# Kernel tuning notes

Hardware: AMD Instinct MI355X
Metric: run time of the kernel (lower is better)

## Reference

```python
import jax, jax.numpy as jnp
import numpy as np

B, H, W, C = 32, 56, 56, 192
WS, SHIFT, HEADS = 7, 3, 6
HID = 4 * C
N = WS * WS
NW = (H // WS) * (W // WS)
EPS = 1e-5


def _rel_index():
    ch, cw = np.meshgrid(np.arange(WS), np.arange(WS), indexing='ij')
    coords = np.stack([ch.ravel(), cw.ravel()])  # [2, N]
    rel = coords[:, :, None] - coords[:, None, :]  # [2, N, N]
    rel = rel.transpose(1, 2, 0)
    rel[:, :, 0] += WS - 1
    rel[:, :, 1] += WS - 1
    rel[:, :, 0] *= 2 * WS - 1
    return rel.sum(-1).astype(np.int32)  # [N, N]


def _attn_mask():
    img = np.zeros((H, W), np.float32)
    sl = (slice(0, -WS), slice(-WS, -SHIFT), slice(-SHIFT, None))
    cnt = 0
    for hs in sl:
        for ws_ in sl:
            img[hs, ws_] = cnt
            cnt += 1
    mw = img.reshape(H // WS, WS, W // WS, WS).transpose(0, 2, 1, 3).reshape(-1, N)
    m = mw[:, None, :] - mw[:, :, None]
    return np.where(m != 0, -100.0, 0.0).astype(np.float32)  # [NW, N, N]


def setup_inputs() -> dict:
    key = jax.random.key(0)
    ks = jax.random.split(key, 16)
    r = lambda k, s, sc: (jax.random.normal(k, s, jnp.float32) * sc)
    return {
        'x': r(ks[0], (B, H * W, C), 1.0),
        'norm1_w': jnp.ones((C,), jnp.float32),
        'norm1_b': jnp.zeros((C,), jnp.float32),
        'qkv_w': r(ks[1], (C, 3 * C), 0.02),
        'qkv_b': jnp.zeros((3 * C,), jnp.float32),
        'bias_table': r(ks[2], ((2 * WS - 1) ** 2, HEADS), 0.02),
        'proj_w': r(ks[3], (C, C), 0.02),
        'proj_b': jnp.zeros((C,), jnp.float32),
        'norm2_w': jnp.ones((C,), jnp.float32),
        'norm2_b': jnp.zeros((C,), jnp.float32),
        'fc1_w': r(ks[4], (C, HID), 0.02),
        'fc1_b': jnp.zeros((HID,), jnp.float32),
        'fc2_w': r(ks[5], (HID, C), 0.02),
        'fc2_b': jnp.zeros((C,), jnp.float32),
        'attn_mask': jnp.asarray(_attn_mask()),
        'rel_index': jnp.asarray(_rel_index()),
    }


def _ln(x, w, b):
    mu = jnp.mean(x, -1, keepdims=True)
    var = jnp.mean(jnp.square(x - mu), -1, keepdims=True)
    return (x - mu) * jax.lax.rsqrt(var + EPS) * w + b


def reference(x, norm1_w, norm1_b, qkv_w, qkv_b, bias_table, proj_w, proj_b,
              norm2_w, norm2_b, fc1_w, fc1_b, fc2_w, fc2_b, attn_mask, rel_index):
    shortcut = x
    h = _ln(x, norm1_w, norm1_b).reshape(B, H, W, C)
    # cyclic shift
    h = jnp.roll(h, shift=(-SHIFT, -SHIFT), axis=(1, 2))
    # window partition -> (B*NW, N, C)
    h = h.reshape(B, H // WS, WS, W // WS, WS, C).transpose(0, 1, 3, 2, 4, 5)
    h = h.reshape(B * NW, N, C)
    # attention
    qkv = (h @ qkv_w + qkv_b).reshape(B * NW, N, 3, HEADS, C // HEADS)
    qkv = qkv.transpose(2, 0, 3, 1, 4)  # [3, B_, heads, N, d]
    q, k, v = qkv[0], qkv[1], qkv[2]
    scale = (C // HEADS) ** -0.5
    attn = jnp.einsum('bhnd,bhmd->bhnm', q * scale, k)
    bias = bias_table[rel_index].transpose(2, 0, 1)  # [heads, N, N]
    attn = attn + bias[None]
    attn = attn.reshape(B, NW, HEADS, N, N) + attn_mask[None, :, None]
    attn = jax.nn.softmax(attn.reshape(B * NW, HEADS, N, N), axis=-1)
    o = jnp.einsum('bhnm,bhmd->bhnd', attn, v)
    o = o.transpose(0, 2, 1, 3).reshape(B * NW, N, C)
    o = o @ proj_w + proj_b
    # window reverse
    o = o.reshape(B, H // WS, W // WS, WS, WS, C).transpose(0, 1, 3, 2, 4, 5)
    o = o.reshape(B, H, W, C)
    o = jnp.roll(o, shift=(SHIFT, SHIFT), axis=(1, 2)).reshape(B, H * W, C)
    x = shortcut + o
    # MLP (exact GELU, like torch nn.GELU)
    m = _ln(x, norm2_w, norm2_b)
    m = jax.nn.gelu(m @ fc1_w + fc1_b, approximate=False) @ fc2_w + fc2_b
    return x + m
```

## Files before the change

kernel.cpp:

```cpp
#include <hip/hip_runtime.h>
#include <math.h>

#define B_    32
#define HH    56
#define WW_   56
#define C_    192
#define WS_   7
#define SHIFT_ 3
#define HEADS_ 6
#define DH    32
#define N_    49
#define NWIN  2048
#define ROWS  100352
#define HID_  768
#define QKVN  576

typedef __bf16 bfr;
typedef __bf16 bf8 __attribute__((ext_vector_type(8)));
typedef __bf16 bf4 __attribute__((ext_vector_type(4)));
typedef float  f32x4 __attribute__((ext_vector_type(4)));

#define MFMA16(a,b,c) __builtin_amdgcn_mfma_f32_16x16x32_bf16(a,b,c,0,0,0)

#define OQW   0
#define OPW   110592
#define OW1   147456
#define OW2   294912
#define OBM   442368
#define WTOT  442368
#define BMTOT 98304

__global__ __launch_bounds__(256) void k_prep(
    const float* __restrict__ qkvw, const float* __restrict__ projw,
    const float* __restrict__ w1,   const float* __restrict__ w2,
    bfr* __restrict__ wsp)
{
  int idx = blockIdx.x*256 + threadIdx.x;
  if (idx >= WTOT) return;
  if (idx < OPW)      { int i=idx;      int n=i/192, k=i%192; wsp[idx] = (bfr)qkvw[k*QKVN + n]; }
  else if (idx < OW1) { int i=idx-OPW;  int n=i/192, k=i%192; wsp[idx] = (bfr)projw[k*C_ + n]; }
  else if (idx < OW2) { int i=idx-OW1;  int n=i/192, k=i%192; wsp[idx] = (bfr)w1[k*HID_ + n]; }
  else                { int i=idx-OW2;  int n=i/768, k=i%768; wsp[idx] = (bfr)w2[k*C_ + n]; }
}

__global__ __launch_bounds__(256) void k_prep2(
    const float* __restrict__ btab, const int* __restrict__ rel,
    const float* __restrict__ mask, bfr* __restrict__ bm)
{
  int idx = blockIdx.x*256 + threadIdx.x;
  if (idx >= BMTOT) return;
  int k = idx & 63, q = (idx>>6) & 63, cls = (idx>>12) & 3, head = idx>>14;
  int wh = (cls & 2) ? 7 : 0, ww = (cls & 1) ? 7 : 0;
  int wi = wh*8 + ww;
  float v = -1e30f;
  if (q < N_ && k < N_) {
    int e = q*N_ + k;
    v = btab[rel[e]*HEADS_ + head] + mask[(size_t)wi*N_*N_ + e];
  }
  bm[idx] = (bfr)v;
}

#define SM_HS 0
#define SM_QS 25600
#define SM_KS 34816
#define SM_VT 44032
#define SM_P  53248
#define SM_OV 62464
#define SM_SR 71680
#define SM1_TOT 71936
#define HSP 200

__global__ __launch_bounds__(256, 2) void k_attn(
    const float* __restrict__ x,
    const float* __restrict__ n1w, const float* __restrict__ n1b,
    const bfr*   __restrict__ wsp,
    const float* __restrict__ qkvb,
    const float* __restrict__ projb,
    float* __restrict__ out)
{
  __shared__ char smem[SM1_TOT];
  bfr*   hs    = (bfr*)(smem + SM_HS);
  bfr*   qs    = (bfr*)(smem + SM_QS);
  bfr*   ks    = (bfr*)(smem + SM_KS);
  bfr*   vT    = (bfr*)(smem + SM_VT);
  bfr*   P     = (bfr*)(smem + SM_P);
  bfr*   ov2   = (bfr*)(smem + SM_OV);
  int*   srows = (int*)(smem + SM_SR);
  float* pj    = (float*)smem;

  const f32x4 ZERO4 = {0.f, 0.f, 0.f, 0.f};

  int win  = blockIdx.x;
  int tid  = threadIdx.x;
  int lane = tid & 63, wave = tid >> 6;
  int ln15 = lane & 15, quad = lane >> 4;
  int wi   = win & 63;
  int cls  = (((wi>>3)==7) ? 2 : 0) + (((wi&7)==7) ? 1 : 0);

  if (tid < N_) {
    int bb = win >> 6;
    int wh = wi >> 3, ww = wi & 7;
    int th = tid / WS_, tw = tid % WS_;
    int sh = wh*WS_ + th + SHIFT_; if (sh >= HH) sh -= HH;
    int sw = ww*WS_ + tw + SHIFT_; if (sw >= WW_) sw -= WW_;
    srows[tid] = bb*HH*WW_ + sh*WW_ + sw;
  }
  {
    int* hz = (int*)(hs + 49*HSP);
    for (int i = tid; i < 15*HSP/2; i += 256) hz[i] = 0;
  }
  __syncthreads();
  for (int r = wave; r < N_; r += 4) {
    const float* xr = x + (size_t)srows[r]*C_;
    float v0 = xr[lane], v1 = xr[lane+64], v2 = xr[lane+128];
    float s = v0+v1+v2, q = v0*v0+v1*v1+v2*v2;
    #pragma unroll
    for (int m = 32; m; m >>= 1) { s += __shfl_xor(s, m); q += __shfl_xor(q, m); }
    float mu = s*(1.f/C_), var = q*(1.f/C_) - mu*mu;
    float rs = rsqrtf(var + 1e-5f);
    hs[r*HSP + lane]     = (bfr)((v0-mu)*rs*n1w[lane]     + n1b[lane]);
    hs[r*HSP + lane+64]  = (bfr)((v1-mu)*rs*n1w[lane+64]  + n1b[lane+64]);
    hs[r*HSP + lane+128] = (bfr)((v2-mu)*rs*n1w[lane+128] + n1b[lane+128]);
  }
  __syncthreads();

  const bfr* qkvwT  = wsp + OQW;
  const bfr* projwT = wsp + OPW;
  const bfr* bmask  = wsp + OBM;

  f32x4 accp[3][4];
  #pragma unroll
  for (int j=0;j<3;j++)
    #pragma unroll
    for (int mt=0;mt<4;mt++) accp[j][mt] = ZERO4;

  for (int pair = 0; pair < 3; pair++) {
    {
      f32x4 qb0 = *(const f32x4*)&qkvb[       pair*64 + wave*16 + quad*4];
      f32x4 qb1 = *(const f32x4*)&qkvb[192  + pair*64 + wave*16 + quad*4];
      float qb2 =                 qkvb[384  + pair*64 + wave*16 + ln15];
      f32x4 acc[3][4];
      #pragma unroll
      for (int j=0;j<3;j++)
        #pragma unroll
        for (int mt=0;mt<4;mt++) acc[j][mt] = ZERO4;
      #pragma unroll
      for (int kk = 0; kk < 6; kk++) {
        bf8 afr[4];
        #pragma unroll
        for (int mt=0;mt<4;mt++)
          afr[mt] = *(const bf8*)&hs[(mt*16+ln15)*HSP + kk*32 + quad*8];
        bf8 bw0 = *(const bf8*)&qkvwT[(size_t)(      pair*64 + wave*16 + ln15)*192 + kk*32 + quad*8];
        bf8 bw1 = *(const bf8*)&qkvwT[(size_t)(192 + pair*64 + wave*16 + ln15)*192 + kk*32 + quad*8];
        bf8 bw2 = *(const bf8*)&qkvwT[(size_t)(384 + pair*64 + wave*16 + ln15)*192 + kk*32 + quad*8];
        #pragma unroll
        for (int mt=0;mt<4;mt++) {
          acc[0][mt] = MFMA16(bw0, afr[mt], acc[0][mt]);
          acc[1][mt] = MFMA16(bw1, afr[mt], acc[1][mt]);
          acc[2][mt] = MFMA16(afr[mt], bw2, acc[2][mt]);
        }
      }
      int hlw = wave >> 1;
      int d0  = (wave & 1)*16 + quad*4;
      int dv  = (wave & 1)*16 + ln15;
      #pragma unroll
      for (int mt=0;mt<4;mt++) {
        int token = mt*16 + ln15;
        bf4 pk;
        #pragma unroll
        for (int r=0;r<4;r++) pk[r] = (bfr)((acc[0][mt][r] + qb0[r])*0.17677669529663689f);
        *(bf4*)&qs[(hlw*64+token)*36 + d0] = pk;
        #pragma unroll
        for (int r=0;r<4;r++) pk[r] = (bfr)(acc[1][mt][r] + qb1[r]);
        *(bf4*)&ks[(hlw*64+token)*36 + d0] = pk;
        #pragma unroll
        for (int r=0;r<4;r++) pk[r] = (bfr)(acc[2][mt][r] + qb2);
        *(bf4*)&vT[(hlw*32+dv)*72 + mt*16 + quad*4] = pk;
      }
    }
    __syncthreads();

    bf4 bm4[2][4];
    #pragma unroll
    for (int hl = 0; hl < 2; hl++) {
      const bfr* bmh = bmask + (((size_t)(pair*2+hl)*4 + cls) << 12);
      #pragma unroll
      for (int nt = 0; nt < 4; nt++)
        bm4[hl][nt] = *(const bf4*)&bmh[(wave*16+ln15)*64 + nt*16 + quad*4];
    }

    float val[2][4][4];
    #pragma unroll
    for (int hl = 0; hl < 2; hl++) {
      bf8 aq = *(const bf8*)&qs[(hl*64 + wave*16 + ln15)*36 + quad*8];
      #pragma unroll
      for (int nt = 0; nt < 4; nt++) {
        f32x4 c;
        c[0] = (float)bm4[hl][nt][0]; c[1] = (float)bm4[hl][nt][1];
        c[2] = (float)bm4[hl][nt][2]; c[3] = (float)bm4[hl][nt][3];
        bf8 bk = *(const bf8*)&ks[(hl*64 + nt*16 + ln15)*36 + quad*8];
        c = MFMA16(bk, aq, c);
        #pragma unroll
        for (int r=0;r<4;r++) val[hl][nt][r] = c[r];
      }
    }

    bf8 pw[2][3];
    #pragma unroll
    for (int hl = 0; hl < 2; hl++)
      #pragma unroll
      for (int j = 0; j < 3; j++)
        pw[hl][j] = *(const bf8*)&projwT[(size_t)((wave*3+j)*16 + ln15)*192
                                         + (pair*2+hl)*32 + quad*8];

    #pragma unroll
    for (int hl = 0; hl < 2; hl++) {
      float mx = val[hl][0][0];
      #pragma unroll
      for (int nt=0;nt<4;nt++)
        #pragma unroll
        for (int r=0;r<4;r++) mx = fmaxf(mx, val[hl][nt][r]);
      mx = fmaxf(mx, __shfl_xor(mx, 16));
      mx = fmaxf(mx, __shfl_xor(mx, 32));
      float sum = 0.f;
      #pragma unroll
      for (int nt=0;nt<4;nt++)
        #pragma unroll
        for (int r=0;r<4;r++) { val[hl][nt][r] = __expf(val[hl][nt][r] - mx); sum += val[hl][nt][r]; }
      sum += __shfl_xor(sum, 16);
      sum += __shfl_xor(sum, 32);
      float rsum = 1.f / sum;
      #pragma unroll
      for (int nt=0;nt<4;nt++) {
        bf4 pk;
        #pragma unroll
        for (int r=0;r<4;r++) pk[r] = (bfr)(val[hl][nt][r]*rsum);
        *(bf4*)&P[(wave*16+ln15)*72 + nt*16 + quad*4] = pk;
      }
      bf8 ap0 = *(const bf8*)&P[(wave*16+ln15)*72 + quad*8];
      bf8 ap1 = *(const bf8*)&P[(wave*16+ln15)*72 + 32 + quad*8];
      #pragma unroll
      for (int nt = 0; nt < 2; nt++) {
        bf8 bv0 = *(const bf8*)&vT[(hl*32 + nt*16 + ln15)*72 + quad*8];
        bf8 bv1 = *(const bf8*)&vT[(hl*32 + nt*16 + ln15)*72 + 32 + quad*8];
        f32x4 c = MFMA16(bv0, ap0, ZERO4);
        c = MFMA16(bv1, ap1, c);
        bf4 pk;
        #pragma unroll
        for (int r=0;r<4;r++) pk[r] = (bfr)c[r];
        *(bf4*)&ov2[(wave*16+ln15)*72 + hl*36 + nt*16 + quad*4] = pk;
      }
    }
    __syncthreads();

    #pragma unroll
    for (int hl = 0; hl < 2; hl++) {
      bf8 afr[4];
      #pragma unroll
      for (int mt=0;mt<4;mt++)
        afr[mt] = *(const bf8*)&ov2[(mt*16+ln15)*72 + hl*36 + quad*8];
      #pragma unroll
      for (int j=0;j<3;j++)
        #pragma unroll
        for (int mt=0;mt<4;mt++) accp[j][mt] = MFMA16(pw[hl][j], afr[mt], accp[j][mt]);
    }
  }

  #pragma unroll
  for (int j=0;j<3;j++) {
    int col0 = (wave*3+j)*16 + quad*4;
    f32x4 pb = *(const f32x4*)&projb[col0];
    #pragma unroll
    for (int mt=0;mt<4;mt++) {
      f32x4 w;
      #pragma unroll
      for (int r=0;r<4;r++) w[r] = accp[j][mt][r] + pb[r];
      *(f32x4*)&pj[(mt*16+ln15)*196 + col0] = w;
    }
  }
  __syncthreads();
  for (int idx = tid; idx < N_*C_; idx += 256) {
    int n = idx / C_, c = idx % C_;
    size_t gr = (size_t)srows[n]*C_ + c;
    out[gr] = x[gr] + pj[n*196 + c];
  }
}

#define SM2_TS  0
#define SM2_HID 25600
#define SM2_TOT 51200

__global__ __launch_bounds__(256, 2) void k_mlp(
    float* __restrict__ y,
    const float* __restrict__ n2w, const float* __restrict__ n2b,
    const bfr* __restrict__ wsp,
    const float* __restrict__ b1, const float* __restrict__ b2)
{
  __shared__ char smem[SM2_TOT];
  bfr*   ts   = (bfr*)(smem + SM2_TS);
  bfr*   hidc = (bfr*)(smem + SM2_HID);
  float* st   = (float*)smem;

  const f32x4 ZERO4 = {0.f, 0.f, 0.f, 0.f};

  int r0 = blockIdx.x * 64;
  int tid = threadIdx.x;
  int lane = tid & 63, wave = tid >> 6;
  int ln15 = lane & 15, quad = lane >> 4;

  #pragma unroll
  for (int i = 0; i < 16; i++) {
    int r = wave + i*4;
    const float* yr = y + (size_t)(r0 + r)*C_;
    float v0 = yr[lane], v1 = yr[lane+64], v2 = yr[lane+128];
    float s = v0+v1+v2, q = v0*v0+v1*v1+v2*v2;
    #pragma unroll
    for (int m = 32; m; m >>= 1) { s += __shfl_xor(s, m); q += __shfl_xor(q, m); }
    float mu = s*(1.f/C_), var = q*(1.f/C_) - mu*mu;
    float rs = rsqrtf(var + 1e-5f);
    ts[r*HSP + lane]     = (bfr)((v0-mu)*rs*n2w[lane]     + n2b[lane]);
    ts[r*HSP + lane+64]  = (bfr)((v1-mu)*rs*n2w[lane+64]  + n2b[lane+64]);
    ts[r*HSP + lane+128] = (bfr)((v2-mu)*rs*n2w[lane+128] + n2b[lane+128]);
  }
  __syncthreads();

  const bfr* w1T = wsp + OW1;
  const bfr* w2T = wsp + OW2;

  f32x4 accp[3][4];
  #pragma unroll
  for (int j=0;j<3;j++)
    #pragma unroll
    for (int mt=0;mt<4;mt++) accp[j][mt] = ZERO4;

  for (int c = 0; c < 4; c++) {
    bf8 wf1[3][6];
    f32x4 bbv[3];
    #pragma unroll
    for (int j=0;j<3;j++) {
      const bfr* wb = w1T + (size_t)((c*12 + wave*3 + j)*16 + ln15)*192 + quad*8;
      #pragma unroll
      for (int kk=0;kk<6;kk++)
        wf1[j][kk] = *(const bf8*)&wb[kk*32];
      bbv[j] = *(const f32x4*)&b1[c*192 + (wave*3+j)*16 + quad*4];
    }
    f32x4 acc[3][4];
    #pragma unroll
    for (int j=0;j<3;j++)
      #pragma unroll
      for (int mt=0;mt<4;mt++) acc[j][mt] = ZERO4;
    #pragma unroll
    for (int kk = 0; kk < 6; kk++) {
      bf8 afr[4];
      #pragma unroll
      for (int mt=0;mt<4;mt++)
        afr[mt] = *(const bf8*)&ts[(mt*16+ln15)*HSP + kk*32 + quad*8];
      #pragma unroll
      for (int j=0;j<3;j++)
        #pragma unroll
        for (int mt=0;mt<4;mt++) acc[j][mt] = MFMA16(wf1[j][kk], afr[mt], acc[j][mt]);
    }
    bf8 wf2[3][6];
    #pragma unroll
    for (int j=0;j<3;j++) {
      const bfr* wb2 = w2T + (size_t)((wave*3+j)*16 + ln15)*768 + c*192 + quad*8;
      #pragma unroll
      for (int kk=0;kk<6;kk++)
        wf2[j][kk] = *(const bf8*)&wb2[kk*32];
      int colc0 = (wave*3 + j)*16 + quad*4;
      #pragma unroll
      for (int mt=0;mt<4;mt++) {
        bf4 pk;
        #pragma unroll
        for (int r=0;r<4;r++) {
          float g = acc[j][mt][r] + bbv[j][r];
          float u = g*(1.5957691216f + 0.0713548170f*g*g);
          pk[r] = (bfr)(g / (1.f + __expf(-u)));
        }
        *(bf4*)&hidc[(mt*16+ln15)*HSP + colc0] = pk;
      }
    }
    __syncthreads();
    #pragma unroll
    for (int kk = 0; kk < 6; kk++) {
      bf8 afr[4];
      #pragma unroll
      for (int mt=0;mt<4;mt++)
        afr[mt] = *(const bf8*)&hidc[(mt*16+ln15)*HSP + kk*32 + quad*8];
      #pragma unroll
      for (int j=0;j<3;j++)
        #pragma unroll
        for (int mt=0;mt<4;mt++) accp[j][mt] = MFMA16(wf2[j][kk], afr[mt], accp[j][mt]);
    }
    __syncthreads();
  }

  #pragma unroll
  for (int j=0;j<3;j++) {
    int col0 = (wave*3+j)*16 + quad*4;
    f32x4 bb2 = *(const f32x4*)&b2[col0];
    #pragma unroll
    for (int mt=0;mt<4;mt++) {
      f32x4 w;
      #pragma unroll
      for (int r=0;r<4;r++) w[r] = accp[j][mt][r] + bb2[r];
      *(f32x4*)&st[(mt*16+ln15)*196 + col0] = w;
    }
  }
  __syncthreads();
  for (int idx = tid; idx < 64*C_; idx += 256) {
    int r = idx / C_, c = idx % C_;
    size_t gr = (size_t)(r0 + r)*C_ + c;
    y[gr] = y[gr] + st[r*196 + c];
  }
}

extern "C" void kernel_launch(void* const* d_in, const int* in_sizes, int n_in,
                              void* d_out, int out_size, void* d_ws, size_t ws_size,
                              hipStream_t stream) {
  const float* x     = (const float*)d_in[0];
  const float* n1w   = (const float*)d_in[1];
  const float* n1b   = (const float*)d_in[2];
  const float* qkvw  = (const float*)d_in[3];
  const float* qkvb  = (const float*)d_in[4];
  const float* btab  = (const float*)d_in[5];
  const float* projw = (const float*)d_in[6];
  const float* projb = (const float*)d_in[7];
  const float* n2w   = (const float*)d_in[8];
  const float* n2b   = (const float*)d_in[9];
  const float* w1    = (const float*)d_in[10];
  const float* b1    = (const float*)d_in[11];
  const float* w2    = (const float*)d_in[12];
  const float* b2    = (const float*)d_in[13];
  const float* mask  = (const float*)d_in[14];
  const int*   rel   = (const int*)d_in[15];
  float* out = (float*)d_out;
  bfr*   wsp = (bfr*)d_ws;

  k_prep<<<(WTOT+255)/256, 256, 0, stream>>>(qkvw, projw, w1, w2, wsp);
  k_prep2<<<(BMTOT+255)/256, 256, 0, stream>>>(btab, rel, mask, wsp + OBM);
  k_attn<<<NWIN, 256, 0, stream>>>(x, n1w, n1b, wsp, qkvb, projb, out);
  k_mlp<<<ROWS/64, 256, 0, stream>>>(out, n2w, n2b, wsp, b1, b2);
}
```

Measured before the change: 533.8 us.

## Cache shortcut rows in registers and stream MLP weights to raise occupancy

The attention kernel now keeps the gathered x rows in registers after LayerNorm and reuses them for the residual add, replacing a second global read of x. The write-back also switches from a strided flat loop to a per-row loop. The MLP kernel stops preloading whole weight fragment arrays into registers and instead loads each bf8 weight fragment right before its MFMAs, and raises launch bounds to 3 blocks per CU. The aim is more occupancy with less register pressure. The risks are extra register pressure in the attention kernel from 39 cached floats per lane, and exposed global-load latency inside the MLP inner loops.

Result: faster. 466.3 us (-12.6%).

```diff
diff --git a/kernel.cpp b/kernel.cpp
--- a/kernel.cpp
+++ b/kernel.cpp
@@ -110,17 +110,23 @@
     for (int i = tid; i < 15*HSP/2; i += 256) hz[i] = 0;
   }
   __syncthreads();
-  for (int r = wave; r < N_; r += 4) {
-    const float* xr = x + (size_t)srows[r]*C_;
-    float v0 = xr[lane], v1 = xr[lane+64], v2 = xr[lane+128];
-    float s = v0+v1+v2, q = v0*v0+v1*v1+v2*v2;
-    #pragma unroll
-    for (int m = 32; m; m >>= 1) { s += __shfl_xor(s, m); q += __shfl_xor(q, m); }
-    float mu = s*(1.f/C_), var = q*(1.f/C_) - mu*mu;
-    float rs = rsqrtf(var + 1e-5f);
-    hs[r*HSP + lane]     = (bfr)((v0-mu)*rs*n1w[lane]     + n1b[lane]);
-    hs[r*HSP + lane+64]  = (bfr)((v1-mu)*rs*n1w[lane+64]  + n1b[lane+64]);
-    hs[r*HSP + lane+128] = (bfr)((v2-mu)*rs*n1w[lane+128] + n1b[lane+128]);
+  float xv0[13], xv1[13], xv2[13];
+  #pragma unroll
+  for (int i = 0; i < 13; i++) {
+    int r = wave + i*4;
+    if (r < N_) {
+      const float* xr = x + (size_t)srows[r]*C_;
+      float v0 = xr[lane], v1 = xr[lane+64], v2 = xr[lane+128];
+      xv0[i] = v0; xv1[i] = v1; xv2[i] = v2;
+      float s = v0+v1+v2, q = v0*v0+v1*v1+v2*v2;
+      #pragma unroll
+      for (int m = 32; m; m >>= 1) { s += __shfl_xor(s, m); q += __shfl_xor(q, m); }
+      float mu = s*(1.f/C_), var = q*(1.f/C_) - mu*mu;
+      float rs = rsqrtf(var + 1e-5f);
+      hs[r*HSP + lane]     = (bfr)((v0-mu)*rs*n1w[lane]     + n1b[lane]);
+      hs[r*HSP + lane+64]  = (bfr)((v1-mu)*rs*n1w[lane+64]  + n1b[lane+64]);
+      hs[r*HSP + lane+128] = (bfr)((v2-mu)*rs*n1w[lane+128] + n1b[lane+128]);
+    }
   }
   __syncthreads();
 
@@ -279,10 +285,15 @@
     }
   }
   __syncthreads();
-  for (int idx = tid; idx < N_*C_; idx += 256) {
-    int n = idx / C_, c = idx % C_;
-    size_t gr = (size_t)srows[n]*C_ + c;
-    out[gr] = x[gr] + pj[n*196 + c];
+  #pragma unroll
+  for (int i = 0; i < 13; i++) {
+    int r = wave + i*4;
+    if (r < N_) {
+      float* orow = out + (size_t)srows[r]*C_;
+      orow[lane]     = xv0[i] + pj[r*196 + lane];
+      orow[lane+64]  = xv1[i] + pj[r*196 + lane+64];
+      orow[lane+128] = xv2[i] + pj[r*196 + lane+128];
+    }
   }
 }
 
@@ -290,7 +301,7 @@
 #define SM2_HID 25600
 #define SM2_TOT 51200
 
-__global__ __launch_bounds__(256, 2) void k_mlp(
+__global__ __launch_bounds__(256, 3) void k_mlp(
     float* __restrict__ y,
     const float* __restrict__ n2w, const float* __restrict__ n2b,
     const bfr* __restrict__ wsp,
@@ -334,16 +345,6 @@
     for (int mt=0;mt<4;mt++) accp[j][mt] = ZERO4;
 
   for (int c = 0; c < 4; c++) {
-    bf8 wf1[3][6];
-    f32x4 bbv[3];
-    #pragma unroll
-    for (int j=0;j<3;j++) {
-      const bfr* wb = w1T + (size_t)((c*12 + wave*3 + j)*16 + ln15)*192 + quad*8;
-      #pragma unroll
-      for (int kk=0;kk<6;kk++)
-        wf1[j][kk] = *(const bf8*)&wb[kk*32];
-      bbv[j] = *(const f32x4*)&b1[c*192 + (wave*3+j)*16 + quad*4];
-    }
     f32x4 acc[3][4];
     #pragma unroll
     for (int j=0;j<3;j++)
@@ -356,24 +357,23 @@
       for (int mt=0;mt<4;mt++)
         afr[mt] = *(const bf8*)&ts[(mt*16+ln15)*HSP + kk*32 + quad*8];
       #pragma unroll
-      for (int j=0;j<3;j++)
-        #pragma unroll
-        for (int mt=0;mt<4;mt++) acc[j][mt] = MFMA16(wf1[j][kk], afr[mt], acc[j][mt]);
-    }
-    bf8 wf2[3][6];
+      for (int j=0;j<3;j++) {
+        bf8 bw = *(const bf8*)&w1T[(size_t)((c*12 + wave*3 + j)*16 + ln15)*192
+                                   + kk*32 + quad*8];
+        #pragma unroll
+        for (int mt=0;mt<4;mt++) acc[j][mt] = MFMA16(bw, afr[mt], acc[j][mt]);
+      }
+    }
     #pragma unroll
     for (int j=0;j<3;j++) {
-      const bfr* wb2 = w2T + (size_t)((wave*3+j)*16 + ln15)*768 + c*192 + quad*8;
-      #pragma unroll
-      for (int kk=0;kk<6;kk++)
-        wf2[j][kk] = *(const bf8*)&wb2[kk*32];
+      f32x4 bbv = *(const f32x4*)&b1[c*192 + (wave*3+j)*16 + quad*4];
       int colc0 = (wave*3 + j)*16 + quad*4;
       #pragma unroll
       for (int mt=0;mt<4;mt++) {
         bf4 pk;
         #pragma unroll
         for (int r=0;r<4;r++) {
-          float g = acc[j][mt][r] + bbv[j][r];
+          float g = acc[j][mt][r] + bbv[r];
           float u = g*(1.5957691216f + 0.0713548170f*g*g);
           pk[r] = (bfr)(g / (1.f + __expf(-u)));
         }
@@ -388,9 +388,12 @@
       for (int mt=0;mt<4;mt++)
         afr[mt] = *(const bf8*)&hidc[(mt*16+ln15)*HSP + kk*32 + quad*8];
       #pragma unroll
-      for (int j=0;j<3;j++)
-        #pragma unroll
-        for (int mt=0;mt<4;mt++) accp[j][mt] = MFMA16(wf2[j][kk], afr[mt], accp[j][mt]);
+      for (int j=0;j<3;j++) {
+        bf8 bw = *(const bf8*)&w2T[(size_t)((wave*3+j)*16 + ln15)*768
+                                   + c*192 + kk*32 + quad*8];
+        #pragma unroll
+        for (int mt=0;mt<4;mt++) accp[j][mt] = MFMA16(bw, afr[mt], accp[j][mt]);
+      }
     }
     __syncthreads();
   }
```
